# Optimization experiments

Measured on AMD Instinct MI355X. Metric: run time of the kernel, lower is better.

## Reference

```python
import jax, jax.numpy as jnp
import numpy as np


def _remove_nan(m, value=0.0):
    # utils.remove_nan: replace NaNs with `value`
    return jnp.where(jnp.isnan(m), jnp.asarray(value, m.dtype), m)


def _gradient(m, axis):
    # roll-based first difference with NaN scrubbing, as in get_gradient
    return _remove_nan(jnp.roll(m, 1, axis=axis) - m)


def setup_inputs() -> dict:
    key = jax.random.key(0)
    x = jax.random.normal(key, (32, 1, 1024, 1024), dtype=jnp.float32)
    return {"x": x}


def reference(x) -> jnp.ndarray:
    # remove_nan(inputs, 1.0) before the map_fn
    x = _remove_nan(x, 1.0)
    # per-element axes 1,2 under map_fn == batched axes 2,3 ([B, C, H, W])
    gx = _gradient(_gradient(x, 2), 2)  # 2nd-order diff along H
    gy = _gradient(_gradient(x, 3), 3)  # 2nd-order diff along W
    g = jnp.clip(gx + gy, -1.0, 1.0) * jnp.asarray(0.5, x.dtype)
    return _remove_nan(g)
```

## Files before the change

### kernel.cpp

```cpp
#include <hip/hip_runtime.h>


#define HH 1024
#define WW 1024

__device__ __forceinline__ float rn1(float v) {
    return (v != v) ? 1.0f : v;
}

__global__ __launch_bounds__(256) void laplacian_kernel(
        const float* __restrict__ x, float* __restrict__ out, int total4) {
    const int stride = gridDim.x * blockDim.x;
    for (int i = blockIdx.x * blockDim.x + threadIdx.x; i < total4; i += stride) {
        const int w4 = i & (WW / 4 - 1);
        const int r  = i >> 8;
        const int h  = r & (HH - 1);
        const int imgBase = (r - h) << 10;
        const float* __restrict__ img = x + imgBase;

        const int w     = w4 << 2;
        const int rowH  = h << 10;
        const int rowM1 = ((h - 1) & (HH - 1)) << 10;
        const int rowM2 = ((h - 2) & (HH - 1)) << 10;

        const float4 cur = *(const float4*)(img + rowH  + w);
        const float4 u1  = *(const float4*)(img + rowM1 + w);
        const float4 u2  = *(const float4*)(img + rowM2 + w);
        const float swm1 = img[rowH + ((w - 1) & (WW - 1))];
        const float swm2 = img[rowH + ((w - 2) & (WW - 1))];

        const float c[6] = { rn1(swm2), rn1(swm1),
                             rn1(cur.x), rn1(cur.y), rn1(cur.z), rn1(cur.w) };
        const float a1[4] = { rn1(u1.x), rn1(u1.y), rn1(u1.z), rn1(u1.w) };
        const float a2[4] = { rn1(u2.x), rn1(u2.y), rn1(u2.z), rn1(u2.w) };

        float4 o;
        float* op = &o.x;
        #pragma unroll
        for (int j = 0; j < 4; ++j) {
            const float gx = a2[j] - 2.0f * a1[j] + c[j + 2];
            const float gy = c[j]  - 2.0f * c[j + 1] + c[j + 2];
            float g = gx + gy;
            g = fminf(fmaxf(g, -1.0f), 1.0f) * 0.5f;
            op[j] = (g != g) ? 0.0f : g;
        }
        *(float4*)(out + imgBase + rowH + w) = o;
    }
}

extern "C" void kernel_launch(void* const* d_in, const int* in_sizes, int n_in,
                              void* d_out, int out_size, void* d_ws, size_t ws_size,
                              hipStream_t stream) {
    const float* x = (const float*)d_in[0];
    float* out = (float*)d_out;
    const int total4 = out_size / 4;
    const int threads = 256;
    const int blocks = 2048;
    laplacian_kernel<<<blocks, threads, 0, stream>>>(x, out, total4);
}
```

Before: 235.2 us.

## Process 8-row strips per block with register row reuse and XCD-aware block mapping

Each block now handles one 8-row strip of one image, and each thread owns one float4 column slot. It loads the 10 vertically needed rows once into registers and reuses them across the strip, where the old grid-stride loop fetched three rows per output. West neighbours come in as one float2 load per row, blocks are remapped so neighbouring strips stay on the same XCD for L2 locality, and outputs use nontemporal stores. The launch geometry is now hard-wired to 32 images of 1024x1024, and register use grows.

```diff
diff --git a/kernel.cpp b/kernel.cpp
--- a/kernel.cpp
+++ b/kernel.cpp
@@ -3,48 +3,63 @@
 
 #define HH 1024
 #define WW 1024
+#define RPB 8
+#define NXCD 8
+
+typedef float f32x4 __attribute__((ext_vector_type(4)));
+typedef float f32x2 __attribute__((ext_vector_type(2)));
 
 __device__ __forceinline__ float rn1(float v) {
     return (v != v) ? 1.0f : v;
 }
 
 __global__ __launch_bounds__(256) void laplacian_kernel(
-        const float* __restrict__ x, float* __restrict__ out, int total4) {
-    const int stride = gridDim.x * blockDim.x;
-    for (int i = blockIdx.x * blockDim.x + threadIdx.x; i < total4; i += stride) {
-        const int w4 = i & (WW / 4 - 1);
-        const int r  = i >> 8;
-        const int h  = r & (HH - 1);
-        const int imgBase = (r - h) << 10;
-        const float* __restrict__ img = x + imgBase;
+        const float* __restrict__ x, float* __restrict__ out) {
+    const int cpx = gridDim.x / NXCD;
+    const int wg  = (blockIdx.x % NXCD) * cpx + blockIdx.x / NXCD;
 
-        const int w     = w4 << 2;
-        const int rowH  = h << 10;
-        const int rowM1 = ((h - 1) & (HH - 1)) << 10;
-        const int rowM2 = ((h - 2) & (HH - 1)) << 10;
+    const int strip = wg & 127;
+    const int img_i = wg >> 7;
+    const int r0    = strip * RPB;
+    const float* __restrict__ img  = x   + ((long)img_i << 20);
+    float*       __restrict__ oimg = out + ((long)img_i << 20);
 
-        const float4 cur = *(const float4*)(img + rowH  + w);
-        const float4 u1  = *(const float4*)(img + rowM1 + w);
-        const float4 u2  = *(const float4*)(img + rowM2 + w);
-        const float swm1 = img[rowH + ((w - 1) & (WW - 1))];
-        const float swm2 = img[rowH + ((w - 2) & (WW - 1))];
+    const int c = threadIdx.x;
+    const int w = c << 2;
 
-        const float c[6] = { rn1(swm2), rn1(swm1),
-                             rn1(cur.x), rn1(cur.y), rn1(cur.z), rn1(cur.w) };
+    f32x4 rowv[RPB + 2];
+    #pragma unroll
+    for (int k = 0; k < RPB + 2; ++k) {
+        const int r = (r0 + k - 2) & (HH - 1);
+        rowv[k] = *(const f32x4*)(img + (r << 10) + w);
+    }
+    f32x2 wp[RPB];
+    const int wm2 = (w - 2) & (WW - 1);
+    #pragma unroll
+    for (int k = 0; k < RPB; ++k) {
+        wp[k] = *(const f32x2*)(img + ((r0 + k) << 10) + wm2);
+    }
+
+    #pragma unroll
+    for (int k = 0; k < RPB; ++k) {
+        const f32x4 cur = rowv[k + 2];
+        const f32x4 u1  = rowv[k + 1];
+        const f32x4 u2  = rowv[k];
+        const float cc[4] = { rn1(cur.x), rn1(cur.y), rn1(cur.z), rn1(cur.w) };
         const float a1[4] = { rn1(u1.x), rn1(u1.y), rn1(u1.z), rn1(u1.w) };
         const float a2[4] = { rn1(u2.x), rn1(u2.y), rn1(u2.z), rn1(u2.w) };
-
-        float4 o;
-        float* op = &o.x;
+        const float west[6] = { rn1(wp[k].x), rn1(wp[k].y),
+                                cc[0], cc[1], cc[2], cc[3] };
+        f32x4 o;
         #pragma unroll
         for (int j = 0; j < 4; ++j) {
-            const float gx = a2[j] - 2.0f * a1[j] + c[j + 2];
-            const float gy = c[j]  - 2.0f * c[j + 1] + c[j + 2];
+            const float gx = a2[j]   - 2.0f * a1[j]       + cc[j];
+            const float gy = west[j] - 2.0f * west[j + 1] + cc[j];
             float g = gx + gy;
             g = fminf(fmaxf(g, -1.0f), 1.0f) * 0.5f;
-            op[j] = (g != g) ? 0.0f : g;
+            o[j] = (g != g) ? 0.0f : g;
         }
-        *(float4*)(out + imgBase + rowH + w) = o;
+        __builtin_nontemporal_store(o, (f32x4*)(oimg + ((r0 + k) << 10) + w));
     }
 }
 
@@ -53,8 +68,6 @@
                               hipStream_t stream) {
     const float* x = (const float*)d_in[0];
     float* out = (float*)d_out;
-    const int total4 = out_size / 4;
-    const int threads = 256;
-    const int blocks = 2048;
-    laplacian_kernel<<<blocks, threads, 0, stream>>>(x, out, total4);
+    const int blocks = 32 * (HH / RPB);
+    laplacian_kernel<<<blocks, 256, 0, stream>>>(x, out);
 }
```

Measured after the change: 241.5 us. +2.6%, slower.
